# Optimization experiments

Hardware: AMD Instinct MI355X
Metric: run time of the kernel (lower is better)

## Reference

```python
import jax, jax.numpy as jnp
import numpy as np

N = 100000
E = 1000000
IN_DIM = 128
HID = 32
HEADS = 4
OUT_DIM = 64
NEG_SLOPE = 0.2


def _gat_layer(x, src, dst, W, a_src, a_dst, b, heads, out_ch, concat):
    n = x.shape[0]
    h = (x @ W).reshape(n, heads, out_ch)                     # [N,H,C]
    s_src = jnp.sum(h * a_src, axis=-1)                        # [N,H]
    s_dst = jnp.sum(h * a_dst, axis=-1)                        # [N,H]
    e = jax.nn.leaky_relu(s_src[src] + s_dst[dst], NEG_SLOPE)  # [E,H]
    # segment softmax over incoming edges of each destination node
    m = jax.ops.segment_max(e, dst, num_segments=n)            # [N,H]
    w = jnp.exp(e - m[dst])                                    # [E,H]
    denom = jax.ops.segment_sum(w, dst, num_segments=n)        # [N,H]
    alpha = w / denom[dst]                                     # [E,H]
    out = jax.ops.segment_sum(h[src] * alpha[:, :, None], dst, num_segments=n)  # [N,H,C]
    out = out.reshape(n, heads * out_ch) if concat else out[:, 0, :]
    return out + b


def setup_inputs() -> dict:
    key = jax.random.key(0)
    ks = jax.random.split(key, 12)
    g = 0.1
    return {
        "x": jax.random.normal(ks[0], (N, IN_DIM), dtype=jnp.float32),
        "edge_index": jax.random.randint(ks[1], (2, E), 0, N, dtype=jnp.int64),
        "W1": jax.random.normal(ks[2], (IN_DIM, HEADS * HID), dtype=jnp.float32) * g,
        "a_src1": jax.random.normal(ks[3], (HEADS, HID), dtype=jnp.float32) * g,
        "a_dst1": jax.random.normal(ks[4], (HEADS, HID), dtype=jnp.float32) * g,
        "b1": jnp.zeros((HEADS * HID,), dtype=jnp.float32),
        "W2": jax.random.normal(ks[5], (HEADS * HID, OUT_DIM), dtype=jnp.float32) * g,
        "a_src2": jax.random.normal(ks[6], (1, OUT_DIM), dtype=jnp.float32) * g,
        "a_dst2": jax.random.normal(ks[7], (1, OUT_DIM), dtype=jnp.float32) * g,
        "b2": jnp.zeros((OUT_DIM,), dtype=jnp.float32),
        "fc_W": jax.random.normal(ks[8], (OUT_DIM, OUT_DIM), dtype=jnp.float32) * g,
        "fc_b": jnp.zeros((OUT_DIM,), dtype=jnp.float32),
    }


def reference(x, edge_index, W1, a_src1, a_dst1, b1, W2, a_src2, a_dst2, b2, fc_W, fc_b):
    # PyG GATConv adds self-loops by default
    loop = jnp.arange(N, dtype=edge_index.dtype)
    src = jnp.concatenate([edge_index[0], loop])
    dst = jnp.concatenate([edge_index[1], loop])
    h = _gat_layer(x, src, dst, W1, a_src1, a_dst1, b1, HEADS, HID, concat=True)
    h = jax.nn.relu(h)
    h = _gat_layer(h, src, dst, W2, a_src2, a_dst2, b2, 1, OUT_DIM, concat=False)
    h = h @ fc_W + fc_b
    return jax.nn.log_softmax(h, axis=1)
```

## Files before the change

### kernel.cpp

```cpp
#include <hip/hip_runtime.h>
#include <hip/hip_bf16.h>
#include <cfloat>

#define NN 100000
#define EE 1000000
#define TE (EE + NN)
#define C1 128
#define C2 64
#define NB1 782
#define NBKT 782
#define BCAP 4096

typedef unsigned short u16;
typedef unsigned int u32;
using bf16x8 = __attribute__((ext_vector_type(8))) short;
using f32x4  = __attribute__((ext_vector_type(4))) float;

__device__ __forceinline__ float lrelu(float v) { return v > 0.f ? v : 0.2f * v; }
__device__ __forceinline__ u16 f2bf(float f) {
    u32 b = __float_as_uint(f);
    b += 0x7fffu + ((b >> 16) & 1u);
    return (u16)(b >> 16);
}
__device__ __forceinline__ float bflo(u32 p) { return __uint_as_float(p << 16); }
__device__ __forceinline__ float bfhi(u32 p) { return __uint_as_float(p & 0xffff0000u); }

__global__ __launch_bounds__(64) void kprep(const float* __restrict__ W2,
    const float* __restrict__ as2, const float* __restrict__ ad2,
    const float* __restrict__ b2, const float* __restrict__ fcW,
    const float* __restrict__ fcb, const float* __restrict__ W1,
    u16* __restrict__ W2pbt, u16* __restrict__ W1bt,
    float* __restrict__ us, float* __restrict__ ud, float* __restrict__ b2p) {
    int b = blockIdx.x, t = threadIdx.x;
    if (b < 128) {
        float s = 0.f;
        for (int k = 0; k < 64; ++k) s = fmaf(W2[b * 64 + k], fcW[k * 64 + t], s);
        W2pbt[t * 128 + b] = f2bf(s);
    } else if (b < 130) {
        int r = (b - 128) * 64 + t;
        float s = 0.f, d = 0.f;
        for (int k = 0; k < 64; ++k) {
            float wv = W2[r * 64 + k];
            s = fmaf(wv, as2[k], s);
            d = fmaf(wv, ad2[k], d);
        }
        us[r] = s; ud[r] = d;
    } else if (b == 130) {
        float s = fcb[t];
        for (int k = 0; k < 64; ++k) s = fmaf(b2[k], fcW[k * 64 + t], s);
        b2p[t] = s;
    } else {
        int c = b - 131;
        W1bt[c * 128 + t]      = f2bf(W1[t * 128 + c]);
        W1bt[c * 128 + 64 + t] = f2bf(W1[(64 + t) * 128 + c]);
    }
}

__global__ __launch_bounds__(256) void kpassA(const int* __restrict__ esrc,
    const int* __restrict__ edst, int* __restrict__ bcnt, u32* __restrict__ bbuf) {
    int i = blockIdx.x * 256 + threadIdx.x;
    if (i >= EE / 4) return;
    int4 s4 = ((const int4*)esrc)[i];
    int4 d4 = ((const int4*)edst)[i];
    int d, s, b, pos;
    d = d4.x; s = s4.x; b = d >> 7;
    pos = atomicAdd(bcnt + b * 16, 1);
    if (pos < BCAP) bbuf[(size_t)b * BCAP + pos] = (u32)s | ((u32)(d & 127) << 17);
    d = d4.y; s = s4.y; b = d >> 7;
    pos = atomicAdd(bcnt + b * 16, 1);
    if (pos < BCAP) bbuf[(size_t)b * BCAP + pos] = (u32)s | ((u32)(d & 127) << 17);
    d = d4.z; s = s4.z; b = d >> 7;
    pos = atomicAdd(bcnt + b * 16, 1);
    if (pos < BCAP) bbuf[(size_t)b * BCAP + pos] = (u32)s | ((u32)(d & 127) << 17);
    d = d4.w; s = s4.w; b = d >> 7;
    pos = atomicAdd(bcnt + b * 16, 1);
    if (pos < BCAP) bbuf[(size_t)b * BCAP + pos] = (u32)s | ((u32)(d & 127) << 17);
}

__global__ __launch_bounds__(1024) void kbscan(const int* __restrict__ bcnt,
                                               int* __restrict__ bbase) {
    __shared__ int sm[1024];
    int t = threadIdx.x;
    int v = 0;
    if (t < NBKT) {
        int node0 = t * 128;
        int nn = NN - node0; if (nn > 128) nn = 128;
        int m = bcnt[t * 16]; if (m > BCAP) m = BCAP;
        v = m + nn;
    }
    sm[t] = v;
    __syncthreads();
    for (int off = 1; off < 1024; off <<= 1) {
        int o = 0;
        if (t >= off) o = sm[t - off];
        __syncthreads();
        if (t >= off) sm[t] += o;
        __syncthreads();
    }
    if (t < NBKT) bbase[t] = sm[t] - v;
}

__global__ __launch_bounds__(256) void kpassB(const int* __restrict__ bcnt,
    const int* __restrict__ bbase, const u32* __restrict__ bbuf,
    int* __restrict__ rowstart, int* __restrict__ eidx) {
    __shared__ int deg[128], lsc[128], cur[128];
    __shared__ int elocal[BCAP + 128];
    int b = blockIdx.x, t = threadIdx.x;
    int node0 = b * 128;
    int nNodes = NN - node0; if (nNodes > 128) nNodes = 128;
    int M = bcnt[b * 16]; if (M > BCAP) M = BCAP;
    int base = bbase[b];
    if (t < 128) deg[t] = 0;
    __syncthreads();
    const u32* bp = bbuf + (size_t)b * BCAP;
    for (int i = t; i < M; i += 256) atomicAdd(&deg[bp[i] >> 17], 1);
    __syncthreads();
    int v = 0;
    if (t < 128) { v = (t < nNodes) ? (1 + deg[t]) : 0; lsc[t] = v; }
    __syncthreads();
    for (int off = 1; off < 128; off <<= 1) {
        int o = 0;
        if (t < 128 && t >= off) o = lsc[t - off];
        __syncthreads();
        if (t < 128 && t >= off) lsc[t] += o;
        __syncthreads();
    }
    if (t < nNodes) {
        int st = lsc[t] - v;
        rowstart[node0 + t] = base + st;
        elocal[st] = node0 + t;
        cur[t] = st + 1;
    }
    if (b == NBKT - 1 && t == 0) rowstart[NN] = TE;
    __syncthreads();
    for (int i = t; i < M; i += 256) {
        u32 p = bp[i];
        int pos = atomicAdd(&cur[p >> 17], 1);
        elocal[pos] = (int)(p & 0x1FFFFu);
    }
    __syncthreads();
    int total = M + nNodes;
    for (int i = t; i < total; i += 256) eidx[base + i] = elocal[i];
}

__global__ __launch_bounds__(256, 1) void k1_mfma(const float* __restrict__ x,
    const u16* __restrict__ W1bt, u16* __restrict__ h1b) {
    __shared__ u16 As[128][136];
    __shared__ u16 Bs[128][136];
    int t = threadIdx.x;
    int rbase = blockIdx.x * 128;
    #pragma unroll
    for (int j = 0; j < 8; ++j) {
        int i = t + 256 * j, row = i >> 4, seg = i & 15;
        *reinterpret_cast<uint4*>(&Bs[row][seg * 8]) =
            *reinterpret_cast<const uint4*>(W1bt + row * 128 + seg * 8);
    }
    #pragma unroll
    for (int j = 0; j < 16; ++j) {
        int i = t + 256 * j, row = i >> 5, c4 = i & 31;
        int gr = rbase + row; if (gr >= NN) gr = NN - 1;
        float4 v = *reinterpret_cast<const float4*>(x + (size_t)gr * 128 + c4 * 4);
        ushort4 o2 = make_ushort4(f2bf(v.x), f2bf(v.y), f2bf(v.z), f2bf(v.w));
        *reinterpret_cast<ushort4*>(&As[row][c4 * 4]) = o2;
    }
    __syncthreads();
    int lane = t & 63, wv = t >> 6, wr = wv >> 1, wc = wv & 1;
    int fr = lane & 15, fg = lane >> 4;
    f32x4 acc[4][4];
    #pragma unroll
    for (int m = 0; m < 4; ++m)
        #pragma unroll
        for (int n = 0; n < 4; ++n) acc[m][n] = (f32x4){0.f, 0.f, 0.f, 0.f};
    #pragma unroll
    for (int kk = 0; kk < 4; ++kk) {
        bf16x8 af[4], bfr[4];
        #pragma unroll
        for (int m = 0; m < 4; ++m)
            af[m] = *reinterpret_cast<const bf16x8*>(&As[wr * 64 + m * 16 + fr][kk * 32 + fg * 8]);
        #pragma unroll
        for (int n = 0; n < 4; ++n)
            bfr[n] = *reinterpret_cast<const bf16x8*>(&Bs[wc * 64 + n * 16 + fr][kk * 32 + fg * 8]);
        #pragma unroll
        for (int m = 0; m < 4; ++m)
            #pragma unroll
            for (int n = 0; n < 4; ++n)
                acc[m][n] = __builtin_amdgcn_mfma_f32_16x16x32_bf16(af[m], bfr[n], acc[m][n], 0, 0, 0);
    }
    #pragma unroll
    for (int m = 0; m < 4; ++m)
        #pragma unroll
        for (int r = 0; r < 4; ++r) {
            int row = rbase + wr * 64 + m * 16 + fg * 4 + r;
            if (row < NN) {
                #pragma unroll
                for (int n = 0; n < 4; ++n)
                    h1b[(size_t)row * 128 + wc * 64 + n * 16 + fr] = f2bf(acc[m][n][r]);
            }
        }
}

__global__ __launch_bounds__(256) void kscore1(const u16* __restrict__ h1b,
    const float* __restrict__ as1, const float* __restrict__ ad1,
    float* __restrict__ ssrc, float* __restrict__ sdst) {
    __shared__ float asl[128], adl[128];
    if (threadIdx.x < 128) { asl[threadIdx.x] = as1[threadIdx.x]; adl[threadIdx.x] = ad1[threadIdx.x]; }
    __syncthreads();
    int g = blockIdx.x * 256 + threadIdx.x;
    if (g >= NN * 4) return;
    int row = g >> 2, h = g & 3;
    const u16* hp = h1b + (size_t)row * 128 + h * 32;
    float ps = 0.f, pd = 0.f;
    #pragma unroll
    for (int q = 0; q < 4; ++q) {
        uint4 pk = *reinterpret_cast<const uint4*>(hp + q * 8);
        u32 wsv[4] = {pk.x, pk.y, pk.z, pk.w};
        #pragma unroll
        for (int e = 0; e < 4; ++e) {
            int c = h * 32 + q * 8 + e * 2;
            float lo = bflo(wsv[e]), hi = bfhi(wsv[e]);
            ps = fmaf(lo, asl[c], ps); ps = fmaf(hi, asl[c + 1], ps);
            pd = fmaf(lo, adl[c], pd); pd = fmaf(hi, adl[c + 1], pd);
        }
    }
    ssrc[g] = ps;
    sdst[g] = pd;
}

__global__ __launch_bounds__(256) void agg1(const int* __restrict__ rowstart,
    const int* __restrict__ eidx, const float* __restrict__ ssrc,
    const float* __restrict__ sdst, const u16* __restrict__ h1b,
    const float* __restrict__ b1, const float* __restrict__ usv,
    const float* __restrict__ udv, u16* __restrict__ hrb,
    float* __restrict__ ssrc2, float* __restrict__ sdst2) {
    int lane = threadIdx.x & 63;
    int n = blockIdx.x * 4 + (threadIdx.x >> 6);
    if (n >= NN) return;
    int r0 = rowstart[n], deg = rowstart[n + 1] - r0;
    int h4 = lane >> 4, j16 = lane & 15;
    int half = lane >> 5, c = lane & 31, hh = c >> 3;
    float sd = sdst[n * 4 + h4];
    int s0 = (j16 < deg) ? eidx[r0 + j16] : eidx[r0];
    uint2 pv[8];
    #pragma unroll
    for (int q = 0; q < 8; ++q) {
        int s = __shfl(s0, 2 * q + half);
        pv[q] = *(const uint2*)(h1b + (size_t)s * C1 + 4 * c);
    }
    float sv0 = (j16 < deg) ? lrelu(ssrc[s0 * 4 + h4] + sd) : -FLT_MAX;
    float mx = sv0;
    #pragma unroll
    for (int off = 1; off <= 8; off <<= 1) mx = fmaxf(mx, __shfl_xor(mx, off));
    for (int base = 16; base < deg; base += 16) {
        int j = base + j16;
        float sv = (j < deg) ? lrelu(ssrc[eidx[r0 + j] * 4 + h4] + sd) : -FLT_MAX;
        #pragma unroll
        for (int off = 1; off <= 8; off <<= 1) sv = fmaxf(sv, __shfl_xor(sv, off));
        mx = fmaxf(mx, sv);
    }
    float w = (j16 < deg) ? __expf(sv0 - mx) : 0.f;
    float den = w;
    float a0 = 0.f, a1 = 0.f, a2 = 0.f, a3 = 0.f;
    #pragma unroll
    for (int q = 0; q < 8; ++q) {
        float wq = __shfl(w, (hh << 4) + 2 * q + half);
        a0 = fmaf(wq, bflo(pv[q].x), a0);
        a1 = fmaf(wq, bfhi(pv[q].x), a1);
        a2 = fmaf(wq, bflo(pv[q].y), a2);
        a3 = fmaf(wq, bfhi(pv[q].y), a3);
    }
    for (int base = 16; base < deg; base += 16) {
        int j = base + j16;
        int sreg = (j < deg) ? eidx[r0 + j] : eidx[r0];
        uint2 qv[8];
        #pragma unroll
        for (int q = 0; q < 8; ++q) {
            int s = __shfl(sreg, 2 * q + half);
            qv[q] = *(const uint2*)(h1b + (size_t)s * C1 + 4 * c);
        }
        float wb = (j < deg) ? __expf(lrelu(ssrc[sreg * 4 + h4] + sd) - mx) : 0.f;
        den += wb;
        #pragma unroll
        for (int q = 0; q < 8; ++q) {
            float wq = __shfl(wb, (hh << 4) + 2 * q + half);
            a0 = fmaf(wq, bflo(qv[q].x), a0);
            a1 = fmaf(wq, bfhi(qv[q].x), a1);
            a2 = fmaf(wq, bflo(qv[q].y), a2);
            a3 = fmaf(wq, bfhi(qv[q].y), a3);
        }
    }
    #pragma unroll
    for (int off = 1; off <= 8; off <<= 1) den += __shfl_xor(den, off);
    float dh = __shfl(den, hh << 4);
    a0 += __shfl_xor(a0, 32);
    a1 += __shfl_xor(a1, 32);
    a2 += __shfl_xor(a2, 32);
    a3 += __shfl_xor(a3, 32);
    float4 bv = *(const float4*)(b1 + 4 * c);
    float rv = 1.f / dh;
    float v0 = fmaf(a0, rv, bv.x); v0 = v0 > 0.f ? v0 : 0.f;
    float v1 = fmaf(a1, rv, bv.y); v1 = v1 > 0.f ? v1 : 0.f;
    float v2 = fmaf(a2, rv, bv.z); v2 = v2 > 0.f ? v2 : 0.f;
    float v3 = fmaf(a3, rv, bv.w); v3 = v3 > 0.f ? v3 : 0.f;
    float4 u_s = *(const float4*)(usv + 4 * c);
    float4 u_d = *(const float4*)(udv + 4 * c);
    float ps = v0 * u_s.x + v1 * u_s.y + v2 * u_s.z + v3 * u_s.w;
    float pd = v0 * u_d.x + v1 * u_d.y + v2 * u_d.z + v3 * u_d.w;
    #pragma unroll
    for (int off = 1; off <= 16; off <<= 1) {
        ps += __shfl_xor(ps, off); pd += __shfl_xor(pd, off);
    }
    if (lane == 0) { ssrc2[n] = ps; sdst2[n] = pd; }
    if (half == 0) {
        ushort4 hs = make_ushort4(f2bf(v0), f2bf(v1), f2bf(v2), f2bf(v3));
        *reinterpret_cast<ushort4*>(hrb + (size_t)n * C1 + 4 * c) = hs;
    }
}

__global__ __launch_bounds__(256, 1) void k5_mfma(const u16* __restrict__ hrb,
    const u16* __restrict__ W2pbt, u16* __restrict__ h3b) {
    __shared__ u16 As[128][136];
    __shared__ u16 Bs[64][136];
    int t = threadIdx.x;
    int rbase = blockIdx.x * 128;
    #pragma unroll
    for (int j = 0; j < 4; ++j) {
        int i = t + 256 * j, row = i >> 4, seg = i & 15;
        *reinterpret_cast<uint4*>(&Bs[row][seg * 8]) =
            *reinterpret_cast<const uint4*>(W2pbt + row * 128 + seg * 8);
    }
    #pragma unroll
    for (int j = 0; j < 8; ++j) {
        int i = t + 256 * j, row = i >> 4, seg = i & 15;
        int gr = rbase + row; if (gr >= NN) gr = NN - 1;
        *reinterpret_cast<uint4*>(&As[row][seg * 8]) =
            *reinterpret_cast<const uint4*>(hrb + (size_t)gr * 128 + seg * 8);
    }
    __syncthreads();
    int lane = t & 63, wv = t >> 6, wr = wv >> 1, wc = wv & 1;
    int fr = lane & 15, fg = lane >> 4;
    f32x4 acc[4][2];
    #pragma unroll
    for (int m = 0; m < 4; ++m)
        #pragma unroll
        for (int n = 0; n < 2; ++n) acc[m][n] = (f32x4){0.f, 0.f, 0.f, 0.f};
    #pragma unroll
    for (int kk = 0; kk < 4; ++kk) {
        bf16x8 af[4], bfr[2];
        #pragma unroll
        for (int m = 0; m < 4; ++m)
            af[m] = *reinterpret_cast<const bf16x8*>(&As[wr * 64 + m * 16 + fr][kk * 32 + fg * 8]);
        #pragma unroll
        for (int n = 0; n < 2; ++n)
            bfr[n] = *reinterpret_cast<const bf16x8*>(&Bs[wc * 32 + n * 16 + fr][kk * 32 + fg * 8]);
        #pragma unroll
        for (int m = 0; m < 4; ++m)
            #pragma unroll
            for (int n = 0; n < 2; ++n)
                acc[m][n] = __builtin_amdgcn_mfma_f32_16x16x32_bf16(af[m], bfr[n], acc[m][n], 0, 0, 0);
    }
    #pragma unroll
    for (int m = 0; m < 4; ++m)
        #pragma unroll
        for (int r = 0; r < 4; ++r) {
            int row = rbase + wr * 64 + m * 16 + fg * 4 + r;
            if (row < NN) {
                #pragma unroll
                for (int n = 0; n < 2; ++n)
                    h3b[(size_t)row * 64 + wc * 32 + n * 16 + fr] = f2bf(acc[m][n][r]);
            }
        }
}

__global__ __launch_bounds__(256) void agg2ls(const int* __restrict__ rowstart,
    const int* __restrict__ eidx, const float* __restrict__ ssrc,
    const float* __restrict__ sdst, const u16* __restrict__ h3b,
    const float* __restrict__ b2p, float* __restrict__ out) {
    int lane = threadIdx.x & 63;
    int n = blockIdx.x * 4 + (threadIdx.x >> 6);
    if (n >= NN) return;
    int r0 = rowstart[n], deg = rowstart[n + 1] - r0;
    int j16 = lane & 15, quarter = lane >> 4, c16 = lane & 15;
    float sd = sdst[n];
    int s0 = (j16 < deg) ? eidx[r0 + j16] : eidx[r0];
    uint2 pv[4];
    #pragma unroll
    for (int q = 0; q < 4; ++q) {
        int s = __shfl(s0, 4 * q + quarter);
        pv[q] = *(const uint2*)(h3b + (size_t)s * C2 + 4 * c16);
    }
    float sv0 = (j16 < deg) ? lrelu(ssrc[s0] + sd) : -FLT_MAX;
    float mx = sv0;
    #pragma unroll
    for (int off = 1; off <= 8; off <<= 1) mx = fmaxf(mx, __shfl_xor(mx, off));
    for (int base = 16; base < deg; base += 16) {
        int j = base + j16;
        float sv = (j < deg) ? lrelu(ssrc[eidx[r0 + j]] + sd) : -FLT_MAX;
        #pragma unroll
        for (int off = 1; off <= 8; off <<= 1) sv = fmaxf(sv, __shfl_xor(sv, off));
        mx = fmaxf(mx, sv);
    }
    float w = (j16 < deg) ? __expf(sv0 - mx) : 0.f;
    float den = w;
    float a0 = 0.f, a1 = 0.f, a2 = 0.f, a3 = 0.f;
    #pragma unroll
    for (int q = 0; q < 4; ++q) {
        float wq = __shfl(w, 4 * q + quarter);
        a0 = fmaf(wq, bflo(pv[q].x), a0);
        a1 = fmaf(wq, bfhi(pv[q].x), a1);
        a2 = fmaf(wq, bflo(pv[q].y), a2);
        a3 = fmaf(wq, bfhi(pv[q].y), a3);
    }
    for (int base = 16; base < deg; base += 16) {
        int j = base + j16;
        int sreg = (j < deg) ? eidx[r0 + j] : eidx[r0];
        uint2 qv[4];
        #pragma unroll
        for (int q = 0; q < 4; ++q) {
            int s = __shfl(sreg, 4 * q + quarter);
            qv[q] = *(const uint2*)(h3b + (size_t)s * C2 + 4 * c16);
        }
        float wb = (j < deg) ? __expf(lrelu(ssrc[sreg] + sd) - mx) : 0.f;
        den += wb;
        #pragma unroll
        for (int q = 0; q < 4; ++q) {
            float wq = __shfl(wb, 4 * q + quarter);
            a0 = fmaf(wq, bflo(qv[q].x), a0);
            a1 = fmaf(wq, bfhi(qv[q].x), a1);
            a2 = fmaf(wq, bflo(qv[q].y), a2);
            a3 = fmaf(wq, bfhi(qv[q].y), a3);
        }
    }
    #pragma unroll
    for (int off = 1; off <= 8; off <<= 1) den += __shfl_xor(den, off);
    a0 += __shfl_xor(a0, 16); a0 += __shfl_xor(a0, 32);
    a1 += __shfl_xor(a1, 16); a1 += __shfl_xor(a1, 32);
    a2 += __shfl_xor(a2, 16); a2 += __shfl_xor(a2, 32);
    a3 += __shfl_xor(a3, 16); a3 += __shfl_xor(a3, 32);
    float4 bv = *(const float4*)(b2p + 4 * c16);
    float rd = 1.f / den;
    float v0 = a0 * rd + bv.x, v1 = a1 * rd + bv.y;
    float v2 = a2 * rd + bv.z, v3 = a3 * rd + bv.w;
    float m4 = fmaxf(fmaxf(v0, v1), fmaxf(v2, v3));
    #pragma unroll
    for (int off = 1; off <= 8; off <<= 1) m4 = fmaxf(m4, __shfl_xor(m4, off));
    float se = __expf(v0 - m4) + __expf(v1 - m4) + __expf(v2 - m4) + __expf(v3 - m4);
    #pragma unroll
    for (int off = 1; off <= 8; off <<= 1) se += __shfl_xor(se, off);
    float lse = m4 + logf(se);
    if (quarter == 0) {
        *(float4*)(out + (size_t)n * C2 + 4 * c16) =
            make_float4(v0 - lse, v1 - lse, v2 - lse, v3 - lse);
    }
}

extern "C" void kernel_launch(void* const* d_in, const int* in_sizes, int n_in,
                              void* d_out, int out_size, void* d_ws, size_t ws_size,
                              hipStream_t stream) {
    const float* x   = (const float*)d_in[0];
    const int*   ei  = (const int*)d_in[1];
    const float* W1  = (const float*)d_in[2];
    const float* as1 = (const float*)d_in[3];
    const float* ad1 = (const float*)d_in[4];
    const float* b1  = (const float*)d_in[5];
    const float* W2  = (const float*)d_in[6];
    const float* as2 = (const float*)d_in[7];
    const float* ad2 = (const float*)d_in[8];
    const float* b2  = (const float*)d_in[9];
    const float* fcW = (const float*)d_in[10];
    const float* fcb = (const float*)d_in[11];
    float* out = (float*)d_out;

    float* ws = (float*)d_ws;
    size_t o = 0;
    u16* h1b   = (u16*)(ws + o); o += (size_t)NN * C1 / 2;
    u16* hrb   = (u16*)(ws + o); o += (size_t)NN * C1 / 2;
    float* ssrc1 = ws + o; o += (size_t)NN * 4;
    float* sdst1 = ws + o; o += (size_t)NN * 4;
    float* ssrc2 = ws + o; o += NN;
    float* sdst2 = ws + o; o += NN;
    float* usv   = ws + o; o += 128;
    float* udv   = ws + o; o += 128;
    float* b2p   = ws + o; o += 64;
    u16* W2pbt = (u16*)(ws + o); o += 64 * 128 / 2;
    u16* W1bt  = (u16*)(ws + o); o += 128 * 128 / 2;
    int* ip = (int*)(ws + o);
    int* bcnt     = ip; ip += NBKT * 16;
    int* bbase    = ip; ip += 1024;
    int* rowstart = ip; ip += NN + 2;
    int* eidx     = ip; ip += TE;
    u32* bbuf     = (u32*)ip; ip += (size_t)NBKT * BCAP;
    u16* h3b = h1b;

    const int* esrc = ei;
    const int* edst = ei + EE;

    hipMemsetAsync(bcnt, 0, (size_t)NBKT * 16 * sizeof(int), stream);

    kprep<<<259, 64, 0, stream>>>(W2, as2, ad2, b2, fcW, fcb, W1,
                                  W2pbt, W1bt, usv, udv, b2p);

    kpassA<<<(EE / 4 + 255) / 256, 256, 0, stream>>>(esrc, edst, bcnt, bbuf);
    kbscan<<<1, 1024, 0, stream>>>(bcnt, bbase);
    kpassB<<<NBKT, 256, 0, stream>>>(bcnt, bbase, bbuf, rowstart, eidx);

    k1_mfma<<<NB1, 256, 0, stream>>>(x, W1bt, h1b);
    kscore1<<<(NN * 4 + 255) / 256, 256, 0, stream>>>(h1b, as1, ad1, ssrc1, sdst1);
    agg1<<<(NN + 3) / 4, 256, 0, stream>>>(rowstart, eidx, ssrc1, sdst1, h1b, b1,
                                           usv, udv, hrb, ssrc2, sdst2);
    k5_mfma<<<NB1, 256, 0, stream>>>(hrb, W2pbt, h3b);
    agg2ls<<<(NN + 3) / 4, 256, 0, stream>>>(rowstart, eidx, ssrc2, sdst2, h3b, b2p, out);
}
```

Baseline: 212.5 us.

## Fuse layer-1 attention score computation into aggregation with online softmax

Removes the separate kscore1 kernel and its ssrc/sdst buffers. agg1 now computes per-head source and destination scores on the fly from the gathered bf16 feature rows, using shuffle reductions. It also replaces the two-pass max-then-accumulate loop with a single-pass online softmax that rescales the accumulators. This saves a kernel launch, a pass over h1b and the second gather of scores, in exchange for extra shuffles, FMAs and exp work per edge.

Measured after the change: 241.8 us. +13.8%, slower.

```diff
diff --git a/kernel.cpp b/kernel.cpp
--- a/kernel.cpp
+++ b/kernel.cpp
@@ -199,104 +199,66 @@
         }
 }
 
-__global__ __launch_bounds__(256) void kscore1(const u16* __restrict__ h1b,
+__global__ __launch_bounds__(256) void agg1(const int* __restrict__ rowstart,
+    const int* __restrict__ eidx, const u16* __restrict__ h1b,
     const float* __restrict__ as1, const float* __restrict__ ad1,
-    float* __restrict__ ssrc, float* __restrict__ sdst) {
-    __shared__ float asl[128], adl[128];
-    if (threadIdx.x < 128) { asl[threadIdx.x] = as1[threadIdx.x]; adl[threadIdx.x] = ad1[threadIdx.x]; }
-    __syncthreads();
-    int g = blockIdx.x * 256 + threadIdx.x;
-    if (g >= NN * 4) return;
-    int row = g >> 2, h = g & 3;
-    const u16* hp = h1b + (size_t)row * 128 + h * 32;
-    float ps = 0.f, pd = 0.f;
-    #pragma unroll
-    for (int q = 0; q < 4; ++q) {
-        uint4 pk = *reinterpret_cast<const uint4*>(hp + q * 8);
-        u32 wsv[4] = {pk.x, pk.y, pk.z, pk.w};
-        #pragma unroll
-        for (int e = 0; e < 4; ++e) {
-            int c = h * 32 + q * 8 + e * 2;
-            float lo = bflo(wsv[e]), hi = bfhi(wsv[e]);
-            ps = fmaf(lo, asl[c], ps); ps = fmaf(hi, asl[c + 1], ps);
-            pd = fmaf(lo, adl[c], pd); pd = fmaf(hi, adl[c + 1], pd);
-        }
-    }
-    ssrc[g] = ps;
-    sdst[g] = pd;
-}
-
-__global__ __launch_bounds__(256) void agg1(const int* __restrict__ rowstart,
-    const int* __restrict__ eidx, const float* __restrict__ ssrc,
-    const float* __restrict__ sdst, const u16* __restrict__ h1b,
     const float* __restrict__ b1, const float* __restrict__ usv,
     const float* __restrict__ udv, u16* __restrict__ hrb,
     float* __restrict__ ssrc2, float* __restrict__ sdst2) {
     int lane = threadIdx.x & 63;
     int n = blockIdx.x * 4 + (threadIdx.x >> 6);
     if (n >= NN) return;
+    int half = lane >> 5, c = lane & 31, j16 = lane & 15;
+    uint2 sfr = *(const uint2*)(h1b + (size_t)n * C1 + 4 * c);
+    float4 asv = *(const float4*)(as1 + 4 * c);
+    float4 adv = *(const float4*)(ad1 + 4 * c);
     int r0 = rowstart[n], deg = rowstart[n + 1] - r0;
-    int h4 = lane >> 4, j16 = lane & 15;
-    int half = lane >> 5, c = lane & 31, hh = c >> 3;
-    float sd = sdst[n * 4 + h4];
-    int s0 = (j16 < deg) ? eidx[r0 + j16] : eidx[r0];
-    uint2 pv[8];
-    #pragma unroll
-    for (int q = 0; q < 8; ++q) {
-        int s = __shfl(s0, 2 * q + half);
-        pv[q] = *(const uint2*)(h1b + (size_t)s * C1 + 4 * c);
-    }
-    float sv0 = (j16 < deg) ? lrelu(ssrc[s0 * 4 + h4] + sd) : -FLT_MAX;
-    float mx = sv0;
-    #pragma unroll
-    for (int off = 1; off <= 8; off <<= 1) mx = fmaxf(mx, __shfl_xor(mx, off));
-    for (int base = 16; base < deg; base += 16) {
-        int j = base + j16;
-        float sv = (j < deg) ? lrelu(ssrc[eidx[r0 + j] * 4 + h4] + sd) : -FLT_MAX;
-        #pragma unroll
-        for (int off = 1; off <= 8; off <<= 1) sv = fmaxf(sv, __shfl_xor(sv, off));
-        mx = fmaxf(mx, sv);
-    }
-    float w = (j16 < deg) ? __expf(sv0 - mx) : 0.f;
-    float den = w;
-    float a0 = 0.f, a1 = 0.f, a2 = 0.f, a3 = 0.f;
-    #pragma unroll
-    for (int q = 0; q < 8; ++q) {
-        float wq = __shfl(w, (hh << 4) + 2 * q + half);
-        a0 = fmaf(wq, bflo(pv[q].x), a0);
-        a1 = fmaf(wq, bfhi(pv[q].x), a1);
-        a2 = fmaf(wq, bflo(pv[q].y), a2);
-        a3 = fmaf(wq, bfhi(pv[q].y), a3);
-    }
-    for (int base = 16; base < deg; base += 16) {
-        int j = base + j16;
-        int sreg = (j < deg) ? eidx[r0 + j] : eidx[r0];
-        uint2 qv[8];
+    float pdh = bflo(sfr.x) * adv.x + bfhi(sfr.x) * adv.y
+              + bflo(sfr.y) * adv.z + bfhi(sfr.y) * adv.w;
+    pdh += __shfl_xor(pdh, 1); pdh += __shfl_xor(pdh, 2); pdh += __shfl_xor(pdh, 4);
+    float m = -FLT_MAX, den = 0.f, a0 = 0.f, a1 = 0.f, a2 = 0.f, a3 = 0.f;
+    for (int base = 0; base < deg; base += 16) {
+        int sj = (base + j16 < deg) ? eidx[r0 + base + j16] : eidx[r0];
+        uint2 pv[8];
         #pragma unroll
         for (int q = 0; q < 8; ++q) {
-            int s = __shfl(sreg, 2 * q + half);
-            qv[q] = *(const uint2*)(h1b + (size_t)s * C1 + 4 * c);
-        }
-        float wb = (j < deg) ? __expf(lrelu(ssrc[sreg * 4 + h4] + sd) - mx) : 0.f;
-        den += wb;
+            int s = __shfl(sj, 2 * q + half);
+            pv[q] = *(const uint2*)(h1b + (size_t)s * C1 + 4 * c);
+        }
+        float x0[8], x1[8], x2[8], x3[8], e[8];
         #pragma unroll
         for (int q = 0; q < 8; ++q) {
-            float wq = __shfl(wb, (hh << 4) + 2 * q + half);
-            a0 = fmaf(wq, bflo(qv[q].x), a0);
-            a1 = fmaf(wq, bfhi(qv[q].x), a1);
-            a2 = fmaf(wq, bflo(qv[q].y), a2);
-            a3 = fmaf(wq, bfhi(qv[q].y), a3);
-        }
-    }
-    #pragma unroll
-    for (int off = 1; off <= 8; off <<= 1) den += __shfl_xor(den, off);
-    float dh = __shfl(den, hh << 4);
+            x0[q] = bflo(pv[q].x); x1[q] = bfhi(pv[q].x);
+            x2[q] = bflo(pv[q].y); x3[q] = bfhi(pv[q].y);
+            float p = x0[q] * asv.x + x1[q] * asv.y + x2[q] * asv.z + x3[q] * asv.w;
+            p += __shfl_xor(p, 1); p += __shfl_xor(p, 2); p += __shfl_xor(p, 4);
+            e[q] = (base + 2 * q + half < deg) ? lrelu(p + pdh) : -FLT_MAX;
+        }
+        float bm = e[0];
+        #pragma unroll
+        for (int q = 1; q < 8; ++q) bm = fmaxf(bm, e[q]);
+        bm = fmaxf(bm, __shfl_xor(bm, 32));
+        float mn = fmaxf(m, bm);
+        float rr = __expf(m - mn);
+        a0 *= rr; a1 *= rr; a2 *= rr; a3 *= rr; den *= rr;
+        m = mn;
+        #pragma unroll
+        for (int q = 0; q < 8; ++q) {
+            float w = __expf(e[q] - m);
+            den += w;
+            a0 = fmaf(w, x0[q], a0);
+            a1 = fmaf(w, x1[q], a1);
+            a2 = fmaf(w, x2[q], a2);
+            a3 = fmaf(w, x3[q], a3);
+        }
+    }
+    den += __shfl_xor(den, 32);
     a0 += __shfl_xor(a0, 32);
     a1 += __shfl_xor(a1, 32);
     a2 += __shfl_xor(a2, 32);
     a3 += __shfl_xor(a3, 32);
     float4 bv = *(const float4*)(b1 + 4 * c);
-    float rv = 1.f / dh;
+    float rv = 1.f / den;
     float v0 = fmaf(a0, rv, bv.x); v0 = v0 > 0.f ? v0 : 0.f;
     float v1 = fmaf(a1, rv, bv.y); v1 = v1 > 0.f ? v1 : 0.f;
     float v2 = fmaf(a2, rv, bv.z); v2 = v2 > 0.f ? v2 : 0.f;
@@ -474,8 +436,6 @@
     size_t o = 0;
     u16* h1b   = (u16*)(ws + o); o += (size_t)NN * C1 / 2;
     u16* hrb   = (u16*)(ws + o); o += (size_t)NN * C1 / 2;
-    float* ssrc1 = ws + o; o += (size_t)NN * 4;
-    float* sdst1 = ws + o; o += (size_t)NN * 4;
     float* ssrc2 = ws + o; o += NN;
     float* sdst2 = ws + o; o += NN;
     float* usv   = ws + o; o += 128;
@@ -504,8 +464,7 @@
     kpassB<<<NBKT, 256, 0, stream>>>(bcnt, bbase, bbuf, rowstart, eidx);
 
     k1_mfma<<<NB1, 256, 0, stream>>>(x, W1bt, h1b);
-    kscore1<<<(NN * 4 + 255) / 256, 256, 0, stream>>>(h1b, as1, ad1, ssrc1, sdst1);
-    agg1<<<(NN + 3) / 4, 256, 0, stream>>>(rowstart, eidx, ssrc1, sdst1, h1b, b1,
+    agg1<<<(NN + 3) / 4, 256, 0, stream>>>(rowstart, eidx, h1b, as1, ad1, b1,
                                            usv, udv, hrb, ssrc2, sdst2);
     k5_mfma<<<NB1, 256, 0, stream>>>(hrb, W2pbt, h3b);
     agg2ls<<<(NN + 3) / 4, 256, 0, stream>>>(rowstart, eidx, ssrc2, sdst2, h3b, b2p, out);
```

## Fuse prep into bucket pass and drop global bucket scan via fixed slots

Applied to the files above, without the earlier changes.

Merges the weight-prep kernel into the edge bucketing kernel as extra blocks and removes the single-block prefix scan by giving each bucket a fixed-size slot in the CSR edge array, storing per-node degrees separately. This cuts two kernel launches and one serialized dependency step. The aggregation kernels now read degree from a separate array, and agg2ls hoists the source-score load earlier. The cost is a padded, non-contiguous edge array and an extra degree-array read.

New measurement: 204.1 us. -4.0%, faster.

```diff
diff --git a/kernel.cpp b/kernel.cpp
--- a/kernel.cpp
+++ b/kernel.cpp
@@ -10,6 +10,8 @@
 #define NB1 782
 #define NBKT 782
 #define BCAP 4096
+#define BSLOT (BCAP + 128)
+#define NPA 977
 
 typedef unsigned short u16;
 typedef unsigned int u32;
@@ -25,13 +27,36 @@
 __device__ __forceinline__ float bflo(u32 p) { return __uint_as_float(p << 16); }
 __device__ __forceinline__ float bfhi(u32 p) { return __uint_as_float(p & 0xffff0000u); }
 
-__global__ __launch_bounds__(64) void kprep(const float* __restrict__ W2,
-    const float* __restrict__ as2, const float* __restrict__ ad2,
-    const float* __restrict__ b2, const float* __restrict__ fcW,
-    const float* __restrict__ fcb, const float* __restrict__ W1,
-    u16* __restrict__ W2pbt, u16* __restrict__ W1bt,
+__global__ __launch_bounds__(256) void kpassA(const int* __restrict__ esrc,
+    const int* __restrict__ edst, int* __restrict__ bcnt, u32* __restrict__ bbuf,
+    const float* __restrict__ W2, const float* __restrict__ as2,
+    const float* __restrict__ ad2, const float* __restrict__ b2,
+    const float* __restrict__ fcW, const float* __restrict__ fcb,
+    const float* __restrict__ W1, u16* __restrict__ W2pbt, u16* __restrict__ W1bt,
     float* __restrict__ us, float* __restrict__ ud, float* __restrict__ b2p) {
-    int b = blockIdx.x, t = threadIdx.x;
+    int blk = blockIdx.x;
+    if (blk < NPA) {
+        int i = blk * 256 + threadIdx.x;
+        if (i >= EE / 4) return;
+        int4 s4 = ((const int4*)esrc)[i];
+        int4 d4 = ((const int4*)edst)[i];
+        int d, s, b, pos;
+        d = d4.x; s = s4.x; b = d >> 7;
+        pos = atomicAdd(bcnt + b * 16, 1);
+        if (pos < BCAP) bbuf[(size_t)b * BCAP + pos] = (u32)s | ((u32)(d & 127) << 17);
+        d = d4.y; s = s4.y; b = d >> 7;
+        pos = atomicAdd(bcnt + b * 16, 1);
+        if (pos < BCAP) bbuf[(size_t)b * BCAP + pos] = (u32)s | ((u32)(d & 127) << 17);
+        d = d4.z; s = s4.z; b = d >> 7;
+        pos = atomicAdd(bcnt + b * 16, 1);
+        if (pos < BCAP) bbuf[(size_t)b * BCAP + pos] = (u32)s | ((u32)(d & 127) << 17);
+        d = d4.w; s = s4.w; b = d >> 7;
+        pos = atomicAdd(bcnt + b * 16, 1);
+        if (pos < BCAP) bbuf[(size_t)b * BCAP + pos] = (u32)s | ((u32)(d & 127) << 17);
+        return;
+    }
+    int b = blk - NPA, t = threadIdx.x;
+    if (t >= 64) return;
     if (b < 128) {
         float s = 0.f;
         for (int k = 0; k < 64; ++k) s = fmaf(W2[b * 64 + k], fcW[k * 64 + t], s);
@@ -56,60 +81,16 @@
     }
 }
 
-__global__ __launch_bounds__(256) void kpassA(const int* __restrict__ esrc,
-    const int* __restrict__ edst, int* __restrict__ bcnt, u32* __restrict__ bbuf) {
-    int i = blockIdx.x * 256 + threadIdx.x;
-    if (i >= EE / 4) return;
-    int4 s4 = ((const int4*)esrc)[i];
-    int4 d4 = ((const int4*)edst)[i];
-    int d, s, b, pos;
-    d = d4.x; s = s4.x; b = d >> 7;
-    pos = atomicAdd(bcnt + b * 16, 1);
-    if (pos < BCAP) bbuf[(size_t)b * BCAP + pos] = (u32)s | ((u32)(d & 127) << 17);
-    d = d4.y; s = s4.y; b = d >> 7;
-    pos = atomicAdd(bcnt + b * 16, 1);
-    if (pos < BCAP) bbuf[(size_t)b * BCAP + pos] = (u32)s | ((u32)(d & 127) << 17);
-    d = d4.z; s = s4.z; b = d >> 7;
-    pos = atomicAdd(bcnt + b * 16, 1);
-    if (pos < BCAP) bbuf[(size_t)b * BCAP + pos] = (u32)s | ((u32)(d & 127) << 17);
-    d = d4.w; s = s4.w; b = d >> 7;
-    pos = atomicAdd(bcnt + b * 16, 1);
-    if (pos < BCAP) bbuf[(size_t)b * BCAP + pos] = (u32)s | ((u32)(d & 127) << 17);
-}
-
-__global__ __launch_bounds__(1024) void kbscan(const int* __restrict__ bcnt,
-                                               int* __restrict__ bbase) {
-    __shared__ int sm[1024];
-    int t = threadIdx.x;
-    int v = 0;
-    if (t < NBKT) {
-        int node0 = t * 128;
-        int nn = NN - node0; if (nn > 128) nn = 128;
-        int m = bcnt[t * 16]; if (m > BCAP) m = BCAP;
-        v = m + nn;
-    }
-    sm[t] = v;
-    __syncthreads();
-    for (int off = 1; off < 1024; off <<= 1) {
-        int o = 0;
-        if (t >= off) o = sm[t - off];
-        __syncthreads();
-        if (t >= off) sm[t] += o;
-        __syncthreads();
-    }
-    if (t < NBKT) bbase[t] = sm[t] - v;
-}
-
 __global__ __launch_bounds__(256) void kpassB(const int* __restrict__ bcnt,
-    const int* __restrict__ bbase, const u32* __restrict__ bbuf,
-    int* __restrict__ rowstart, int* __restrict__ eidx) {
+    const u32* __restrict__ bbuf, int* __restrict__ rowstart,
+    int* __restrict__ degs, int* __restrict__ eidx) {
     __shared__ int deg[128], lsc[128], cur[128];
     __shared__ int elocal[BCAP + 128];
     int b = blockIdx.x, t = threadIdx.x;
     int node0 = b * 128;
     int nNodes = NN - node0; if (nNodes > 128) nNodes = 128;
     int M = bcnt[b * 16]; if (M > BCAP) M = BCAP;
-    int base = bbase[b];
+    int base = b * BSLOT;
     if (t < 128) deg[t] = 0;
     __syncthreads();
     const u32* bp = bbuf + (size_t)b * BCAP;
@@ -128,10 +109,10 @@
     if (t < nNodes) {
         int st = lsc[t] - v;
         rowstart[node0 + t] = base + st;
+        degs[node0 + t] = v;
         elocal[st] = node0 + t;
         cur[t] = st + 1;
     }
-    if (b == NBKT - 1 && t == 0) rowstart[NN] = TE;
     __syncthreads();
     for (int i = t; i < M; i += 256) {
         u32 p = bp[i];
@@ -227,15 +208,15 @@
 }
 
 __global__ __launch_bounds__(256) void agg1(const int* __restrict__ rowstart,
-    const int* __restrict__ eidx, const float* __restrict__ ssrc,
-    const float* __restrict__ sdst, const u16* __restrict__ h1b,
-    const float* __restrict__ b1, const float* __restrict__ usv,
-    const float* __restrict__ udv, u16* __restrict__ hrb,
-    float* __restrict__ ssrc2, float* __restrict__ sdst2) {
+    const int* __restrict__ degs, const int* __restrict__ eidx,
+    const float* __restrict__ ssrc, const float* __restrict__ sdst,
+    const u16* __restrict__ h1b, const float* __restrict__ b1,
+    const float* __restrict__ usv, const float* __restrict__ udv,
+    u16* __restrict__ hrb, float* __restrict__ ssrc2, float* __restrict__ sdst2) {
     int lane = threadIdx.x & 63;
     int n = blockIdx.x * 4 + (threadIdx.x >> 6);
     if (n >= NN) return;
-    int r0 = rowstart[n], deg = rowstart[n + 1] - r0;
+    int r0 = rowstart[n], deg = degs[n];
     int h4 = lane >> 4, j16 = lane & 15;
     int half = lane >> 5, c = lane & 31, hh = c >> 3;
     float sd = sdst[n * 4 + h4];
@@ -372,29 +353,32 @@
 }
 
 __global__ __launch_bounds__(256) void agg2ls(const int* __restrict__ rowstart,
-    const int* __restrict__ eidx, const float* __restrict__ ssrc,
-    const float* __restrict__ sdst, const u16* __restrict__ h3b,
-    const float* __restrict__ b2p, float* __restrict__ out) {
+    const int* __restrict__ degs, const int* __restrict__ eidx,
+    const float* __restrict__ ssrc, const float* __restrict__ sdst,
+    const u16* __restrict__ h3b, const float* __restrict__ b2p,
+    float* __restrict__ out) {
     int lane = threadIdx.x & 63;
     int n = blockIdx.x * 4 + (threadIdx.x >> 6);
     if (n >= NN) return;
-    int r0 = rowstart[n], deg = rowstart[n + 1] - r0;
+    int r0 = rowstart[n], deg = degs[n];
     int j16 = lane & 15, quarter = lane >> 4, c16 = lane & 15;
     float sd = sdst[n];
     int s0 = (j16 < deg) ? eidx[r0 + j16] : eidx[r0];
+    float sraw = ssrc[s0];
     uint2 pv[4];
     #pragma unroll
     for (int q = 0; q < 4; ++q) {
         int s = __shfl(s0, 4 * q + quarter);
         pv[q] = *(const uint2*)(h3b + (size_t)s * C2 + 4 * c16);
     }
-    float sv0 = (j16 < deg) ? lrelu(ssrc[s0] + sd) : -FLT_MAX;
+    float sv0 = (j16 < deg) ? lrelu(sraw + sd) : -FLT_MAX;
     float mx = sv0;
     #pragma unroll
     for (int off = 1; off <= 8; off <<= 1) mx = fmaxf(mx, __shfl_xor(mx, off));
     for (int base = 16; base < deg; base += 16) {
         int j = base + j16;
-        float sv = (j < deg) ? lrelu(ssrc[eidx[r0 + j]] + sd) : -FLT_MAX;
+        float sv = -FLT_MAX;
+        if (j < deg) sv = lrelu(ssrc[eidx[r0 + j]] + sd);
         #pragma unroll
         for (int off = 1; off <= 8; off <<= 1) sv = fmaxf(sv, __shfl_xor(sv, off));
         mx = fmaxf(mx, sv);
@@ -413,13 +397,14 @@
     for (int base = 16; base < deg; base += 16) {
         int j = base + j16;
         int sreg = (j < deg) ? eidx[r0 + j] : eidx[r0];
+        float wsr = ssrc[sreg];
         uint2 qv[4];
         #pragma unroll
         for (int q = 0; q < 4; ++q) {
             int s = __shfl(sreg, 4 * q + quarter);
             qv[q] = *(const uint2*)(h3b + (size_t)s * C2 + 4 * c16);
         }
-        float wb = (j < deg) ? __expf(lrelu(ssrc[sreg] + sd) - mx) : 0.f;
+        float wb = (j < deg) ? __expf(lrelu(wsr + sd) - mx) : 0.f;
         den += wb;
         #pragma unroll
         for (int q = 0; q < 4; ++q) {
@@ -485,9 +470,9 @@
     u16* W1bt  = (u16*)(ws + o); o += 128 * 128 / 2;
     int* ip = (int*)(ws + o);
     int* bcnt     = ip; ip += NBKT * 16;
-    int* bbase    = ip; ip += 1024;
     int* rowstart = ip; ip += NN + 2;
-    int* eidx     = ip; ip += TE;
+    int* degs     = ip; ip += NN;
+    int* eidx     = ip; ip += (size_t)NBKT * BSLOT;
     u32* bbuf     = (u32*)ip; ip += (size_t)NBKT * BCAP;
     u16* h3b = h1b;
 
@@ -496,17 +481,16 @@
 
     hipMemsetAsync(bcnt, 0, (size_t)NBKT * 16 * sizeof(int), stream);
 
-    kprep<<<259, 64, 0, stream>>>(W2, as2, ad2, b2, fcW, fcb, W1,
-                                  W2pbt, W1bt, usv, udv, b2p);
-
-    kpassA<<<(EE / 4 + 255) / 256, 256, 0, stream>>>(esrc, edst, bcnt, bbuf);
-    kbscan<<<1, 1024, 0, stream>>>(bcnt, bbase);
-    kpassB<<<NBKT, 256, 0, stream>>>(bcnt, bbase, bbuf, rowstart, eidx);
+    kpassA<<<NPA + 259, 256, 0, stream>>>(esrc, edst, bcnt, bbuf,
+                                          W2, as2, ad2, b2, fcW, fcb, W1,
+                                          W2pbt, W1bt, usv, udv, b2p);
+    kpassB<<<NBKT, 256, 0, stream>>>(bcnt, bbuf, rowstart, degs, eidx);
 
     k1_mfma<<<NB1, 256, 0, stream>>>(x, W1bt, h1b);
     kscore1<<<(NN * 4 + 255) / 256, 256, 0, stream>>>(h1b, as1, ad1, ssrc1, sdst1);
-    agg1<<<(NN + 3) / 4, 256, 0, stream>>>(rowstart, eidx, ssrc1, sdst1, h1b, b1,
-                                           usv, udv, hrb, ssrc2, sdst2);
+    agg1<<<(NN + 3) / 4, 256, 0, stream>>>(rowstart, degs, eidx, ssrc1, sdst1, h1b,
+                                           b1, usv, udv, hrb, ssrc2, sdst2);
     k5_mfma<<<NB1, 256, 0, stream>>>(hrb, W2pbt, h3b);
-    agg2ls<<<(NN + 3) / 4, 256, 0, stream>>>(rowstart, eidx, ssrc2, sdst2, h3b, b2p, out);
-}
+    agg2ls<<<(NN + 3) / 4, 256, 0, stream>>>(rowstart, degs, eidx, ssrc2, sdst2,
+                                             h3b, b2p, out);
+}
```
